# Kernel tuning notes

Measured on AMD Instinct MI355X. Metric: run time of the kernel, lower is better.

## Reference

```python
import jax, jax.numpy as jnp
import numpy as np

B, H, W, C = 2, 128, 128, 256
D = 64          # attention_dim
NH = 1          # num_heads
P = 18          # num_random_points
N = H * W
EPS = 1e-5


def _layernorm(x, gamma, beta):
    mu = jnp.mean(x, axis=-1, keepdims=True)
    var = jnp.var(x, axis=-1, keepdims=True)
    return (x - mu) * jax.lax.rsqrt(var + EPS) * gamma + beta


def setup_inputs() -> dict:
    key = jax.random.key(0)
    ks = jax.random.split(key, 12)
    s = 0.02
    inp = {
        "X": jax.random.normal(ks[0], (B, H, W, C), dtype=jnp.float32),
        "selected_indices": jax.random.randint(ks[1], (B, N, P), 0, N),
        "topk": 1,
        "pos_enc": jax.random.normal(ks[2], (1, H, W, C), dtype=jnp.float32),
        "Wq": jax.random.normal(ks[3], (C, NH * D), dtype=jnp.float32) * s,
        "bq": jnp.zeros((NH * D,), dtype=jnp.float32),
        "Wk": jax.random.normal(ks[4], (C, NH * D), dtype=jnp.float32) * s,
        "bk": jnp.zeros((NH * D,), dtype=jnp.float32),
        "Wv": jax.random.normal(ks[5], (C, NH * D), dtype=jnp.float32) * s,
        "bv": jnp.zeros((NH * D,), dtype=jnp.float32),
        "Wo": jax.random.normal(ks[6], (NH * D, C), dtype=jnp.float32) * s,
        "bo": jnp.zeros((C,), dtype=jnp.float32),
        "W1": jax.random.normal(ks[7], (C, 4 * C), dtype=jnp.float32) * s,
        "b1": jnp.zeros((4 * C,), dtype=jnp.float32),
        "W2": jax.random.normal(ks[8], (4 * C, C), dtype=jnp.float32) * s,
        "b2": jnp.zeros((C,), dtype=jnp.float32),
        "g1": jnp.ones((C,), dtype=jnp.float32),
        "be1": jnp.zeros((C,), dtype=jnp.float32),
        "g2": jnp.ones((C,), dtype=jnp.float32),
        "be2": jnp.zeros((C,), dtype=jnp.float32),
    }
    return inp


def reference(X, selected_indices, topk, pos_enc, Wq, bq, Wk, bk, Wv, bv,
              Wo, bo, W1, b1, W2, b2, g1, be1, g2, be2):
    # forward_wotopk path (topk == 1)
    Xp = X + pos_enc                                  # [B,H,W,C]
    Q = (Xp @ Wq + bq).reshape(B, N, NH, D)
    K = (Xp @ Wk + bk).reshape(B, N, NH, D)
    V = (Xp @ Wv + bv).reshape(B, N, NH, D)

    # gather 18 random K/V rows per query pixel: [B,N,P,NH,D]
    gather = jax.vmap(lambda kv, idx: kv[idx])        # per-batch fancy index
    Ksel = gather(K, selected_indices)
    Vsel = gather(V, selected_indices)

    scores = jnp.einsum('bihd,bijhd->bijh', Q, Ksel) / jnp.sqrt(
        jnp.asarray(D, dtype=jnp.float32))
    attn = jax.nn.softmax(scores, axis=2)             # softmax over the P points
    ctx = jnp.einsum('bijh,bijhd->bihd', attn, Vsel).reshape(B, N, NH * D)

    out = (ctx @ Wo + bo).reshape(B, H, W, C)
    Xn = _layernorm(Xp + out, g1, be1)
    ffn = jax.nn.relu(Xn @ W1 + b1) @ W2 + b2
    out2 = _layernorm(Xn + ffn, g2, be2)
    return out2, attn
```

## Files before the change

kernel.cpp:

```cpp
#include <hip/hip_runtime.h>
#include <hip/hip_bf16.h>

#define CC 256
#define DD 64
#define PP 18
#define ROWS 32768
#define EPSF 1e-5f

typedef __attribute__((ext_vector_type(8))) short bf16x8;
typedef __attribute__((ext_vector_type(4))) short s16x4;
typedef __attribute__((ext_vector_type(4))) float f32x4;

#define BAR_LDS() do {                                        \
    asm volatile("s_waitcnt lgkmcnt(0)" ::: "memory");        \
    __builtin_amdgcn_s_barrier();                             \
    __builtin_amdgcn_sched_barrier(0);                        \
} while (0)

__global__ __launch_bounds__(256) void k_prep(
    const float* __restrict__ Wq, const float* __restrict__ Wk,
    const float* __restrict__ Wv, const float* __restrict__ Wo,
    const float* __restrict__ W1, const float* __restrict__ W2,
    __hip_bfloat16* __restrict__ WqP, __hip_bfloat16* __restrict__ WkP,
    __hip_bfloat16* __restrict__ WvP, __hip_bfloat16* __restrict__ WoP,
    __hip_bfloat16* __restrict__ W1T, __hip_bfloat16* __restrict__ W2T) {
    __shared__ float tile[32][33];
    const int b = blockIdx.x, t = threadIdx.x;
    if (b < 256) {
        int i = b * 256 + t;
        const float* src; __hip_bfloat16* dst; int K, N, j;
        if (i < 16384)      { src = Wq; dst = WqP; K = 256; N = 64;  j = i; }
        else if (i < 32768) { src = Wk; dst = WkP; K = 256; N = 64;  j = i - 16384; }
        else if (i < 49152) { src = Wv; dst = WvP; K = 256; N = 64;  j = i - 32768; }
        else                { src = Wo; dst = WoP; K = 64;  N = 256; j = i - 49152; }
        int e = j & 7, l = (j >> 3) & 63, rest = j >> 9;
        int KS = K >> 5;
        int ks = rest % KS, nt = rest / KS;
        int row = ks * 32 + (l >> 4) * 8 + e;
        int col = nt * 16 + (l & 15);
        dst[j] = __float2bfloat16(src[(long)row * N + col]);
        return;
    }
    const float* src; __hip_bfloat16* dst; int Nsrc, r0, c0, mode;
    if (b < 512) {
        int bb = b - 256;
        r0 = (bb >> 5) * 32; c0 = (bb & 31) * 32;
        src = W1; dst = W1T; Nsrc = 1024; mode = 0;
    } else {
        int bb = b - 512;
        r0 = (bb >> 3) * 32; c0 = (bb & 7) * 32;
        src = W2; dst = W2T; Nsrc = 256; mode = 1;
    }
#pragma unroll
    for (int i = 0; i < 4; ++i) {
        int idx = t + i * 256;
        int r = idx >> 5, c = idx & 31;
        tile[r][c] = src[(long)(r0 + r) * Nsrc + c0 + c];
    }
    __syncthreads();
#pragma unroll
    for (int i = 0; i < 4; ++i) {
        int idx = t + i * 256;
        int c2 = idx >> 5, r2 = idx & 31;
        long doff = (mode == 0) ? ((long)(c0 + c2) * 256 + r0 + r2)
                                : ((long)(c0 + c2) * 1024 + r0 + r2);
        dst[doff] = __float2bfloat16(tile[r2][c2]);
    }
}

__global__ __launch_bounds__(256) void k_qkv(
    const float4* __restrict__ X4, const float4* __restrict__ pe4,
    const __hip_bfloat16* __restrict__ WqP, const __hip_bfloat16* __restrict__ WkP,
    const __hip_bfloat16* __restrict__ WvP,
    const float* __restrict__ bq, const float* __restrict__ bk,
    const float* __restrict__ bv,
    __hip_bfloat16* __restrict__ Xpb,
    __hip_bfloat16* __restrict__ Qb, __hip_bfloat16* __restrict__ Kb,
    __hip_bfloat16* __restrict__ Vb) {
    __shared__ short Xs[32 * 256];
    const int t = threadIdx.x, w = t >> 6, l = t & 63;
    const int l15 = l & 15, lh = l >> 4;
    const int row0 = blockIdx.x * 32;

    for (int j = t; j < 2048; j += 256) {
        int r = j >> 6, c4 = j & 63;
        long g = row0 + r;
        float4 a = X4[(g << 6) + c4];
        float4 p = pe4[(long)((g & 16383) << 6) + c4];
        union { s16x4 v; __hip_bfloat16 h[4]; } u;
        u.h[0] = __float2bfloat16(a.x + p.x);
        u.h[1] = __float2bfloat16(a.y + p.y);
        u.h[2] = __float2bfloat16(a.z + p.z);
        u.h[3] = __float2bfloat16(a.w + p.w);
        int db = (r << 9) + (c4 << 3);
        db ^= (r & 7) << 4;
        *(s16x4*)((char*)Xs + db) = u.v;
        *(s16x4*)((char*)Xpb + (g << 9) + (c4 << 3)) = u.v;
    }
    __syncthreads();

    bf16x8 af[2][8];
#pragma unroll
    for (int ri = 0; ri < 2; ++ri)
#pragma unroll
        for (int ks = 0; ks < 8; ++ks) {
            int r = ri * 16 + l15;
            int db = (r << 9) + ks * 64 + lh * 16;
            db ^= (r & 7) << 4;
            af[ri][ks] = *(const bf16x8*)((const char*)Xs + db);
        }

    f32x4 acc[3][2];
#pragma unroll
    for (int j = 0; j < 3; ++j)
#pragma unroll
        for (int ri = 0; ri < 2; ++ri) acc[j][ri] = (f32x4)(0.f);

#pragma unroll
    for (int ks = 0; ks < 8; ++ks)
#pragma unroll
        for (int j = 0; j < 3; ++j) {
            int nt = w * 3 + j;
            const __hip_bfloat16* WP = (nt < 4) ? WqP : ((nt < 8) ? WkP : WvP);
            int ntl = nt & 3;
            bf16x8 b = *(const bf16x8*)(WP + (long)(((ntl * 8 + ks) << 6) + l) * 8);
#pragma unroll
            for (int ri = 0; ri < 2; ++ri)
                acc[j][ri] = __builtin_amdgcn_mfma_f32_16x16x32_bf16(
                    af[ri][ks], b, acc[j][ri], 0, 0, 0);
        }

#pragma unroll
    for (int j = 0; j < 3; ++j) {
        int nt = w * 3 + j;
        __hip_bfloat16* OP = (nt < 4) ? Qb : ((nt < 8) ? Kb : Vb);
        const float* BP = (nt < 4) ? bq : ((nt < 8) ? bk : bv);
        int col = (nt & 3) * 16 + l15;
        float bias = BP[col];
#pragma unroll
        for (int ri = 0; ri < 2; ++ri)
#pragma unroll
            for (int rg = 0; rg < 4; ++rg) {
                long row = row0 + ri * 16 + lh * 4 + rg;
                OP[row * DD + col] = __float2bfloat16(acc[j][ri][rg] + bias);
            }
    }
}

__global__ __launch_bounds__(256) void k_attn(const __hip_bfloat16* __restrict__ Q,
                                              const __hip_bfloat16* __restrict__ K,
                                              const __hip_bfloat16* __restrict__ V,
                                              const int* __restrict__ sel,
                                              __hip_bfloat16* __restrict__ ctx,
                                              float* __restrict__ attn_out) {
    const int wave  = threadIdx.x >> 6;
    const int lane  = threadIdx.x & 63;
    const int token = blockIdx.x * 4 + wave;
    const int b     = token >> 14;
    const int g = lane >> 3, s = lane & 7;

    const int* selp = sel + (long)token * PP;
    int sel_l = (lane < PP) ? selp[lane] : 0;

    float qf[8];
    {
        uint4 qv = *(const uint4*)(Q + (long)token * DD + s * 8);
        qf[0] = __uint_as_float(qv.x << 16);
        qf[1] = __uint_as_float(qv.x & 0xffff0000u);
        qf[2] = __uint_as_float(qv.y << 16);
        qf[3] = __uint_as_float(qv.y & 0xffff0000u);
        qf[4] = __uint_as_float(qv.z << 16);
        qf[5] = __uint_as_float(qv.z & 0xffff0000u);
        qf[6] = __uint_as_float(qv.w << 16);
        qf[7] = __uint_as_float(qv.w & 0xffff0000u);
    }

    const __hip_bfloat16* Kbase = K + (((long)b << 14) * DD);
    float sc[3];
    int idxs[3];
#pragma unroll
    for (int i = 0; i < 3; ++i) {
        int r = i * 8 + g;
        idxs[i] = __shfl(sel_l, r);
        uint4 kv = *(const uint4*)(Kbase + (long)idxs[i] * DD + s * 8);
        float part;
        part = qf[0] * __uint_as_float(kv.x << 16);
        part = fmaf(qf[1], __uint_as_float(kv.x & 0xffff0000u), part);
        part = fmaf(qf[2], __uint_as_float(kv.y << 16), part);
        part = fmaf(qf[3], __uint_as_float(kv.y & 0xffff0000u), part);
        part = fmaf(qf[4], __uint_as_float(kv.z << 16), part);
        part = fmaf(qf[5], __uint_as_float(kv.z & 0xffff0000u), part);
        part = fmaf(qf[6], __uint_as_float(kv.w << 16), part);
        part = fmaf(qf[7], __uint_as_float(kv.w & 0xffff0000u), part);
        part += __shfl_xor(part, 1);
        part += __shfl_xor(part, 2);
        part += __shfl_xor(part, 4);
        sc[i] = (r < PP) ? part * 0.125f : -1e30f;
    }

    float m = fmaxf(fmaxf(sc[0], sc[1]), sc[2]);
    m = fmaxf(m, __shfl_xor(m, 8));
    m = fmaxf(m, __shfl_xor(m, 16));
    m = fmaxf(m, __shfl_xor(m, 32));
    const float L2E = 1.4426950408889634f;
    float e0 = exp2f((sc[0] - m) * L2E);
    float e1 = exp2f((sc[1] - m) * L2E);
    float e2 = exp2f((sc[2] - m) * L2E);
    float dsum = e0 + e1 + e2;
    dsum += __shfl_xor(dsum, 8);
    dsum += __shfl_xor(dsum, 16);
    dsum += __shfl_xor(dsum, 32);
    float inv = 1.f / dsum;

    {
        int srcl = (lane & 7) << 3;
        float b0 = __shfl(e0, srcl);
        float b1 = __shfl(e1, srcl);
        float b2 = __shfl(e2, srcl);
        if (lane < PP) {
            float ev = (lane < 8) ? b0 : ((lane < 16) ? b1 : b2);
            attn_out[(long)token * PP + lane] = ev * inv;
        }
    }

    const __hip_bfloat16* Vbase = V + (((long)b << 14) * DD);
    float ca[8];
#pragma unroll
    for (int j = 0; j < 8; ++j) ca[j] = 0.f;
    float ev3[3] = {e0, e1, e2};
#pragma unroll
    for (int i = 0; i < 3; ++i) {
        uint4 vv = *(const uint4*)(Vbase + (long)idxs[i] * DD + s * 8);
        float e = ev3[i];
        ca[0] = fmaf(e, __uint_as_float(vv.x << 16), ca[0]);
        ca[1] = fmaf(e, __uint_as_float(vv.x & 0xffff0000u), ca[1]);
        ca[2] = fmaf(e, __uint_as_float(vv.y << 16), ca[2]);
        ca[3] = fmaf(e, __uint_as_float(vv.y & 0xffff0000u), ca[3]);
        ca[4] = fmaf(e, __uint_as_float(vv.z << 16), ca[4]);
        ca[5] = fmaf(e, __uint_as_float(vv.z & 0xffff0000u), ca[5]);
        ca[6] = fmaf(e, __uint_as_float(vv.w << 16), ca[6]);
        ca[7] = fmaf(e, __uint_as_float(vv.w & 0xffff0000u), ca[7]);
    }
#pragma unroll
    for (int o = 8; o <= 32; o <<= 1)
#pragma unroll
        for (int j = 0; j < 8; ++j) ca[j] += __shfl_xor(ca[j], o);
    if (g == 0) {
        union { bf16x8 v; __hip_bfloat16 h[8]; } u;
#pragma unroll
        for (int j = 0; j < 8; ++j) u.h[j] = __float2bfloat16(ca[j] * inv);
        *(bf16x8*)(ctx + (long)token * DD + s * 8) = u.v;
    }
}

__global__ __launch_bounds__(256) void k_projln(
    const __hip_bfloat16* __restrict__ ctx, const __hip_bfloat16* __restrict__ WoP,
    const float* __restrict__ bo, const float* __restrict__ g1,
    const float* __restrict__ be1,
    const __hip_bfloat16* __restrict__ Xpb, __hip_bfloat16* __restrict__ Xnb) {
    __shared__ short Cs[32 * 64];
    __shared__ float red[2][32][2];
    __shared__ float mrs[32][2];
    const int t = threadIdx.x, w = t >> 6, l = t & 63;
    const int l15 = l & 15, lh = l >> 4;
    const int row0 = blockIdx.x * 32;

    {
        int r = t >> 3, ch = t & 7;
        int db = (r << 7) + (ch << 4);
        db ^= (r & 7) << 4;
        *(bf16x8*)((char*)Cs + db) = *(const bf16x8*)(ctx + (long)(row0 + r) * DD + ch * 8);
    }
    __syncthreads();

    const int ri = w & 1, nh = w >> 1;

    bf16x8 af[2];
#pragma unroll
    for (int ks = 0; ks < 2; ++ks) {
        int r = ri * 16 + l15;
        int db = (r << 7) + ks * 64 + lh * 16;
        db ^= (r & 7) << 4;
        af[ks] = *(const bf16x8*)((const char*)Cs + db);
    }

    f32x4 acc[8];
#pragma unroll
    for (int j = 0; j < 8; ++j) acc[j] = (f32x4)(0.f);

#pragma unroll
    for (int ks = 0; ks < 2; ++ks)
#pragma unroll
        for (int j = 0; j < 8; ++j) {
            int nt = nh * 8 + j;
            bf16x8 b = *(const bf16x8*)(WoP + (long)(((nt * 2 + ks) << 6) + l) * 8);
            acc[j] = __builtin_amdgcn_mfma_f32_16x16x32_bf16(af[ks], b, acc[j], 0, 0, 0);
        }

    float bov[8], g1v[8], be1v[8];
#pragma unroll
    for (int j = 0; j < 8; ++j) {
        int col = (nh * 8 + j) * 16 + l15;
        bov[j] = bo[col]; g1v[j] = g1[col]; be1v[j] = be1[col];
    }

    float xv[4][8];
#pragma unroll
    for (int rg = 0; rg < 4; ++rg) {
        long grow = row0 + ri * 16 + lh * 4 + rg;
        float s = 0.f, q = 0.f;
#pragma unroll
        for (int j = 0; j < 8; ++j) {
            float v = acc[j][rg] + bov[j] +
                      __bfloat162float(Xpb[grow * CC + (nh * 8 + j) * 16 + l15]);
            xv[rg][j] = v; s += v; q += v * v;
        }
#pragma unroll
        for (int o = 8; o > 0; o >>= 1) { s += __shfl_xor(s, o); q += __shfl_xor(q, o); }
        if (l15 == 0) {
            int rl = ri * 16 + lh * 4 + rg;
            red[nh][rl][0] = s; red[nh][rl][1] = q;
        }
    }
    __syncthreads();
    if (t < 32) {
        float S = red[0][t][0] + red[1][t][0];
        float Q = red[0][t][1] + red[1][t][1];
        float mu = S * (1.f / CC);
        float var = Q * (1.f / CC) - mu * mu;
        mrs[t][0] = mu; mrs[t][1] = rsqrtf(var + EPSF);
    }
    __syncthreads();
#pragma unroll
    for (int rg = 0; rg < 4; ++rg) {
        int rl = ri * 16 + lh * 4 + rg;
        long grow = row0 + rl;
        float mu = mrs[rl][0], rs = mrs[rl][1];
#pragma unroll
        for (int j = 0; j < 8; ++j)
            Xnb[grow * CC + (nh * 8 + j) * 16 + l15] =
                __float2bfloat16((xv[rg][j] - mu) * rs * g1v[j] + be1v[j]);
    }
}

template<int KD, int NDIM, int GRL2, int CTL2>
__global__ __launch_bounds__(256) void k_gemm(
    const __hip_bfloat16* __restrict__ A,
    const __hip_bfloat16* __restrict__ BT,
    const float* __restrict__ bias,
    __hip_bfloat16* __restrict__ Cout) {
    __shared__ short As[4096];
    __shared__ short Bs[4096];

    const int t = threadIdx.x, w = t >> 6, l = t & 63;
    const int l15 = l & 15, lh = l >> 4;
    const int bid = blockIdx.x;
    const int wi = bid & ((1 << (GRL2 + CTL2)) - 1);
    const int rt = ((bid >> (GRL2 + CTL2)) << GRL2) | (wi & ((1 << GRL2) - 1));
    const int ct = wi >> GRL2;
    const int row0 = rt * 128, n0 = ct * 128;
    const int wr = w & 1, wc = w >> 1;

    const int ar = t >> 2;
    const int ak = (t & 3) << 3;
    const int dbase = (ar * 64 + ((t & 3) << 4)) ^ ((ar & 7) << 4);
    const __hip_bfloat16* Ap = A + (long)(row0 + ar) * KD + ak;
    const __hip_bfloat16* Bp = BT + (long)(n0 + ar) * KD + ak;

    bf16x8 ra0 = *(const bf16x8*)(Ap);
    bf16x8 ra1 = *(const bf16x8*)(Ap + (long)64 * KD);
    bf16x8 rb0 = *(const bf16x8*)(Bp);
    bf16x8 rb1 = *(const bf16x8*)(Bp + (long)64 * KD);

    int offA[4], offB[4];
#pragma unroll
    for (int f = 0; f < 4; ++f) {
        int rowA = wr * 64 + f * 16 + l15;
        offA[f] = (rowA * 64 + lh * 16) ^ ((rowA & 7) << 4);
        int rowB = wc * 64 + f * 16 + l15;
        offB[f] = (rowB * 64 + lh * 16) ^ ((rowB & 7) << 4);
    }

    f32x4 acc[4][4];
#pragma unroll
    for (int i = 0; i < 4; ++i)
#pragma unroll
        for (int j = 0; j < 4; ++j) acc[i][j] = (f32x4)(0.f);

    constexpr int KS = KD / 32;
#pragma unroll 1
    for (int ks = 0; ks < KS; ++ks) {
        BAR_LDS();
        *(bf16x8*)((char*)As + dbase)        = ra0;
        *(bf16x8*)((char*)As + 4096 + dbase) = ra1;
        *(bf16x8*)((char*)Bs + dbase)        = rb0;
        *(bf16x8*)((char*)Bs + 4096 + dbase) = rb1;
        if (ks + 1 < KS) {
            const __hip_bfloat16* Ap2 = Ap + (ks + 1) * 32;
            const __hip_bfloat16* Bp2 = Bp + (ks + 1) * 32;
            ra0 = *(const bf16x8*)(Ap2);
            ra1 = *(const bf16x8*)(Ap2 + (long)64 * KD);
            rb0 = *(const bf16x8*)(Bp2);
            rb1 = *(const bf16x8*)(Bp2 + (long)64 * KD);
        }
        BAR_LDS();
        bf16x8 af[4], bfr[4];
#pragma unroll
        for (int f = 0; f < 4; ++f)
            af[f] = *(const bf16x8*)((const char*)As + offA[f]);
#pragma unroll
        for (int f = 0; f < 4; ++f)
            bfr[f] = *(const bf16x8*)((const char*)Bs + offB[f]);
#pragma unroll
        for (int fr = 0; fr < 4; ++fr)
#pragma unroll
            for (int fc = 0; fc < 4; ++fc)
                acc[fr][fc] = __builtin_amdgcn_mfma_f32_16x16x32_bf16(
                    af[fr], bfr[fc], acc[fr][fc], 0, 0, 0);
    }

#pragma unroll
    for (int fc = 0; fc < 4; ++fc) {
        int col = n0 + wc * 64 + fc * 16 + l15;
        float bv = bias[col];
#pragma unroll
        for (int fr = 0; fr < 4; ++fr)
#pragma unroll
            for (int rg = 0; rg < 4; ++rg) {
                int row = wr * 64 + fr * 16 + lh * 4 + rg;
                long gi = (long)(row0 + row) * NDIM + col;
                Cout[gi] = __float2bfloat16(fmaxf(acc[fr][fc][rg] + bv, 0.f));
            }
    }
}

__global__ __launch_bounds__(512) void k_gemm2ln(
    const __hip_bfloat16* __restrict__ A,
    const __hip_bfloat16* __restrict__ BT,
    const float* __restrict__ b2,
    const __hip_bfloat16* __restrict__ Res,
    const float* __restrict__ g2, const float* __restrict__ be2,
    float* __restrict__ out) {
    __shared__ short As[64 * 32];
    __shared__ short Bs[256 * 32];
    __shared__ float red[4][64][2];
    __shared__ float mrs[64][2];

    const int t = threadIdx.x, w = t >> 6, l = t & 63;
    const int l15 = l & 15, lh = l >> 4;
    const int wr = w >> 2, wc = w & 3;
    const int row0 = blockIdx.x * 64;
    const bool doA = (t < 256);

    const int ak = (t & 3) << 3;
    const int dbA  = ((t >> 2) * 64 + ((t & 3) << 4)) ^ (((t >> 2) & 7) << 4);
    const int brB0 = t >> 2;
    const int brB1 = brB0 + 128;
    const int dbB0 = (brB0 * 64 + ((t & 3) << 4)) ^ ((brB0 & 7) << 4);
    const int dbB1 = (brB1 * 64 + ((t & 3) << 4)) ^ ((brB1 & 7) << 4);
    const __hip_bfloat16* Ap  = A  + (long)(row0 + (t >> 2)) * 1024 + ak;
    const __hip_bfloat16* Bp0 = BT + (long)brB0 * 1024 + ak;
    const __hip_bfloat16* Bp1 = BT + (long)brB1 * 1024 + ak;

    bf16x8 ra;
    if (doA) ra = *(const bf16x8*)(Ap);
    bf16x8 rb0 = *(const bf16x8*)(Bp0);
    bf16x8 rb1 = *(const bf16x8*)(Bp1);

    int offA[2], offB[4];
#pragma unroll
    for (int f = 0; f < 2; ++f) {
        int rowA = wr * 32 + f * 16 + l15;
        offA[f] = (rowA * 64 + lh * 16) ^ ((rowA & 7) << 4);
    }
#pragma unroll
    for (int f = 0; f < 4; ++f) {
        int rowB = wc * 64 + f * 16 + l15;
        offB[f] = (rowB * 64 + lh * 16) ^ ((rowB & 7) << 4);
    }

    f32x4 acc[2][4];
#pragma unroll
    for (int i = 0; i < 2; ++i)
#pragma unroll
        for (int j = 0; j < 4; ++j) acc[i][j] = (f32x4)(0.f);

#pragma unroll 1
    for (int ks = 0; ks < 32; ++ks) {
        BAR_LDS();
        if (doA) *(bf16x8*)((char*)As + dbA) = ra;
        *(bf16x8*)((char*)Bs + dbB0) = rb0;
        *(bf16x8*)((char*)Bs + dbB1) = rb1;
        if (ks + 1 < 32) {
            if (doA) ra = *(const bf16x8*)(Ap + (ks + 1) * 32);
            rb0 = *(const bf16x8*)(Bp0 + (ks + 1) * 32);
            rb1 = *(const bf16x8*)(Bp1 + (ks + 1) * 32);
        }
        BAR_LDS();
        bf16x8 af[2], bfr[4];
#pragma unroll
        for (int f = 0; f < 2; ++f)
            af[f] = *(const bf16x8*)((const char*)As + offA[f]);
#pragma unroll
        for (int f = 0; f < 4; ++f)
            bfr[f] = *(const bf16x8*)((const char*)Bs + offB[f]);
#pragma unroll
        for (int fr = 0; fr < 2; ++fr)
#pragma unroll
            for (int fc = 0; fc < 4; ++fc)
                acc[fr][fc] = __builtin_amdgcn_mfma_f32_16x16x32_bf16(
                    af[fr], bfr[fc], acc[fr][fc], 0, 0, 0);
    }

    float b2v[4], g2v[4], be2v[4];
#pragma unroll
    for (int fc = 0; fc < 4; ++fc) {
        int col = wc * 64 + fc * 16 + l15;
        b2v[fc] = b2[col]; g2v[fc] = g2[col]; be2v[fc] = be2[col];
    }
#pragma unroll
    for (int fr = 0; fr < 2; ++fr)
#pragma unroll
        for (int rg = 0; rg < 4; ++rg) {
            int row = wr * 32 + fr * 16 + lh * 4 + rg;
            float s = 0.f, q = 0.f;
#pragma unroll
            for (int fc = 0; fc < 4; ++fc) {
                long gi = (long)(row0 + row) * CC + wc * 64 + fc * 16 + l15;
                float v = acc[fr][fc][rg] + b2v[fc] + __bfloat162float(Res[gi]);
                acc[fr][fc][rg] = v;
                s += v; q += v * v;
            }
#pragma unroll
            for (int o = 8; o > 0; o >>= 1) {
                s += __shfl_xor(s, o); q += __shfl_xor(q, o);
            }
            if (l15 == 0) { red[wc][row][0] = s; red[wc][row][1] = q; }
        }
    __syncthreads();
    if (t < 64) {
        float S = 0.f, Q = 0.f;
#pragma unroll
        for (int ww = 0; ww < 4; ++ww) { S += red[ww][t][0]; Q += red[ww][t][1]; }
        float mu = S * (1.f / CC);
        float var = Q * (1.f / CC) - mu * mu;
        mrs[t][0] = mu; mrs[t][1] = rsqrtf(var + EPSF);
    }
    __syncthreads();
#pragma unroll
    for (int fr = 0; fr < 2; ++fr)
#pragma unroll
        for (int rg = 0; rg < 4; ++rg) {
            int row = wr * 32 + fr * 16 + lh * 4 + rg;
            float mu = mrs[row][0], rs = mrs[row][1];
#pragma unroll
            for (int fc = 0; fc < 4; ++fc) {
                long gi = (long)(row0 + row) * CC + wc * 64 + fc * 16 + l15;
                out[gi] = (acc[fr][fc][rg] - mu) * rs * g2v[fc] + be2v[fc];
            }
        }
}

extern "C" void kernel_launch(void* const* d_in, const int* in_sizes, int n_in,
                              void* d_out, int out_size, void* d_ws, size_t ws_size,
                              hipStream_t stream) {
    const float* X   = (const float*)d_in[0];
    const int*   sel = (const int*)d_in[1];
    const float* pe  = (const float*)d_in[3];
    const float* Wq  = (const float*)d_in[4];
    const float* bq  = (const float*)d_in[5];
    const float* Wk  = (const float*)d_in[6];
    const float* bk  = (const float*)d_in[7];
    const float* Wv  = (const float*)d_in[8];
    const float* bv  = (const float*)d_in[9];
    const float* Wo  = (const float*)d_in[10];
    const float* bo  = (const float*)d_in[11];
    const float* W1  = (const float*)d_in[12];
    const float* b1  = (const float*)d_in[13];
    const float* W2  = (const float*)d_in[14];
    const float* b2  = (const float*)d_in[15];
    const float* g1  = (const float*)d_in[16];
    const float* be1 = (const float*)d_in[17];
    const float* g2  = (const float*)d_in[18];
    const float* be2 = (const float*)d_in[19];

    float* out = (float*)d_out;
    char*  ws  = (char*)d_ws;

    __hip_bfloat16* Xpb = (__hip_bfloat16*)(ws);
    __hip_bfloat16* Qb  = (__hip_bfloat16*)(ws + (16 << 20));
    __hip_bfloat16* Kb  = (__hip_bfloat16*)(ws + (20 << 20));
    __hip_bfloat16* Vb  = (__hip_bfloat16*)(ws + (24 << 20));
    __hip_bfloat16* ctxb= (__hip_bfloat16*)(ws + (28 << 20));
    __hip_bfloat16* H   = (__hip_bfloat16*)(ws + (16 << 20));
    __hip_bfloat16* WqP = (__hip_bfloat16*)(ws + (96 << 20));
    __hip_bfloat16* WkP = WqP + 16384;
    __hip_bfloat16* WvP = WkP + 16384;
    __hip_bfloat16* WoP = WvP + 16384;
    __hip_bfloat16* W1T = WoP + 16384;
    __hip_bfloat16* W2T = W1T + 262144;
    float* attn_out = out + (long)ROWS * CC;

    k_prep<<<768, 256, 0, stream>>>(Wq, Wk, Wv, Wo, W1, W2,
                                    WqP, WkP, WvP, WoP, W1T, W2T);

    k_qkv<<<ROWS / 32, 256, 0, stream>>>((const float4*)X, (const float4*)pe,
                                         WqP, WkP, WvP, bq, bk, bv,
                                         Xpb, Qb, Kb, Vb);

    k_attn<<<ROWS / 4, 256, 0, stream>>>(Qb, Kb, Vb, sel, ctxb, attn_out);

    k_projln<<<ROWS / 32, 256, 0, stream>>>(ctxb, WoP, bo, g1, be1, Xpb, Xpb);

    k_gemm<256, 1024, 3, 3><<<2048, 256, 0, stream>>>(Xpb, W1T, b1, H);
    k_gemm2ln<<<512, 512, 0, stream>>>(H, W2T, b2, Xpb, g2, be2, out);
}
```

Measured before the change: 119.5 us.

## Use direct global-to-LDS loads with double-buffered pipeline in FFN GEMMs

Replaces the register-staged global loads and LDS stores in the two FFN GEMM kernels with global_load_lds (direct-to-LDS DMA) into a two-stage LDS ring. Prefetch runs two K-steps ahead and is synchronised with vmcnt waits instead of two LDS barriers per step. An inverse swizzle maps each lane's LDS destination back to its global source so the existing XOR-swizzled fragment reads keep working. The aim is to drop the VGPR staging and LDS write instructions and to overlap memory with MFMA work. In exchange it doubles LDS use, which may lower occupancy, and it depends on correct vmcnt accounting.

```diff
diff --git a/kernel.cpp b/kernel.cpp
--- a/kernel.cpp
+++ b/kernel.cpp
@@ -16,6 +16,26 @@
     __builtin_amdgcn_s_barrier();                             \
     __builtin_amdgcn_sched_barrier(0);                        \
 } while (0)
+
+#define WAIT_VM(N) do {                                       \
+    asm volatile("s_waitcnt vmcnt(" #N ")" ::: "memory");     \
+    __builtin_amdgcn_s_barrier();                             \
+    __builtin_amdgcn_sched_barrier(0);                        \
+} while (0)
+
+__device__ __forceinline__ void gl_lds16(const void* g, void* l) {
+    __builtin_amdgcn_global_load_lds(
+        (const __attribute__((address_space(1))) unsigned int*)g,
+        (__attribute__((address_space(3))) unsigned int*)l, 16, 0, 0);
+}
+
+__device__ __forceinline__ void inv_swz(int p, int& r, int& c) {
+    int rhi = p >> 7;
+    int r2  = (rhi >> 1) & 1;
+    int r0  = ((p >> 6) & 1) ^ r2;
+    r = (rhi << 1) | r0;
+    c = ((p >> 4) & 3) ^ (r & 3);
+}
 
 __global__ __launch_bounds__(256) void k_prep(
     const float* __restrict__ Wq, const float* __restrict__ Wk,
@@ -349,8 +369,8 @@
     const __hip_bfloat16* __restrict__ BT,
     const float* __restrict__ bias,
     __hip_bfloat16* __restrict__ Cout) {
-    __shared__ short As[4096];
-    __shared__ short Bs[4096];
+    __shared__ short As[2][4096];
+    __shared__ short Bs[2][4096];
 
     const int t = threadIdx.x, w = t >> 6, l = t & 63;
     const int l15 = l & 15, lh = l >> 4;
@@ -361,16 +381,17 @@
     const int row0 = rt * 128, n0 = ct * 128;
     const int wr = w & 1, wc = w >> 1;
 
-    const int ar = t >> 2;
-    const int ak = (t & 3) << 3;
-    const int dbase = (ar * 64 + ((t & 3) << 4)) ^ ((ar & 7) << 4);
-    const __hip_bfloat16* Ap = A + (long)(row0 + ar) * KD + ak;
-    const __hip_bfloat16* Bp = BT + (long)(n0 + ar) * KD + ak;
-
-    bf16x8 ra0 = *(const bf16x8*)(Ap);
-    bf16x8 ra1 = *(const bf16x8*)(Ap + (long)64 * KD);
-    bf16x8 rb0 = *(const bf16x8*)(Bp);
-    bf16x8 rb1 = *(const bf16x8*)(Bp + (long)64 * KD);
+    const __hip_bfloat16* gA[2];
+    const __hip_bfloat16* gB[2];
+#pragma unroll
+    for (int j = 0; j < 2; ++j) {
+        int r, c;
+        inv_swz(j * 4096 + t * 16, r, c);
+        gA[j] = A  + (long)(row0 + r) * KD + c * 8;
+        gB[j] = BT + (long)(n0 + r) * KD + c * 8;
+    }
+    char* ldsA = (char*)As + w * 1024;
+    char* ldsB = (char*)Bs + w * 1024;
 
     int offA[4], offB[4];
 #pragma unroll
@@ -388,35 +409,41 @@
         for (int j = 0; j < 4; ++j) acc[i][j] = (f32x4)(0.f);
 
     constexpr int KS = KD / 32;
+#pragma unroll
+    for (int n = 0; n < 2; ++n)
+#pragma unroll
+        for (int j = 0; j < 2; ++j) {
+            gl_lds16(gA[j] + n * 32, ldsA + n * 8192 + j * 4096);
+            gl_lds16(gB[j] + n * 32, ldsB + n * 8192 + j * 4096);
+        }
+
 #pragma unroll 1
     for (int ks = 0; ks < KS; ++ks) {
-        BAR_LDS();
-        *(bf16x8*)((char*)As + dbase)        = ra0;
-        *(bf16x8*)((char*)As + 4096 + dbase) = ra1;
-        *(bf16x8*)((char*)Bs + dbase)        = rb0;
-        *(bf16x8*)((char*)Bs + 4096 + dbase) = rb1;
-        if (ks + 1 < KS) {
-            const __hip_bfloat16* Ap2 = Ap + (ks + 1) * 32;
-            const __hip_bfloat16* Bp2 = Bp + (ks + 1) * 32;
-            ra0 = *(const bf16x8*)(Ap2);
-            ra1 = *(const bf16x8*)(Ap2 + (long)64 * KD);
-            rb0 = *(const bf16x8*)(Bp2);
-            rb1 = *(const bf16x8*)(Bp2 + (long)64 * KD);
-        }
-        BAR_LDS();
+        if (ks + 1 < KS) { WAIT_VM(4); } else { WAIT_VM(0); }
+        const char* as = (const char*)As + (ks & 1) * 8192;
+        const char* bs = (const char*)Bs + (ks & 1) * 8192;
         bf16x8 af[4], bfr[4];
 #pragma unroll
         for (int f = 0; f < 4; ++f)
-            af[f] = *(const bf16x8*)((const char*)As + offA[f]);
+            af[f] = *(const bf16x8*)(as + offA[f]);
 #pragma unroll
         for (int f = 0; f < 4; ++f)
-            bfr[f] = *(const bf16x8*)((const char*)Bs + offB[f]);
+            bfr[f] = *(const bf16x8*)(bs + offB[f]);
 #pragma unroll
         for (int fr = 0; fr < 4; ++fr)
 #pragma unroll
             for (int fc = 0; fc < 4; ++fc)
                 acc[fr][fc] = __builtin_amdgcn_mfma_f32_16x16x32_bf16(
                     af[fr], bfr[fc], acc[fr][fc], 0, 0, 0);
+        BAR_LDS();
+        if (ks + 2 < KS) {
+            int n = ks + 2;
+#pragma unroll
+            for (int j = 0; j < 2; ++j) {
+                gl_lds16(gA[j] + n * 32, ldsA + (ks & 1) * 8192 + j * 4096);
+                gl_lds16(gB[j] + n * 32, ldsB + (ks & 1) * 8192 + j * 4096);
+            }
+        }
     }
 
 #pragma unroll
@@ -441,8 +468,8 @@
     const __hip_bfloat16* __restrict__ Res,
     const float* __restrict__ g2, const float* __restrict__ be2,
     float* __restrict__ out) {
-    __shared__ short As[64 * 32];
-    __shared__ short Bs[256 * 32];
+    __shared__ short As[2][2048];
+    __shared__ short Bs[2][8192];
     __shared__ float red[4][64][2];
     __shared__ float mrs[64][2];
 
@@ -452,20 +479,21 @@
     const int row0 = blockIdx.x * 64;
     const bool doA = (t < 256);
 
-    const int ak = (t & 3) << 3;
-    const int dbA  = ((t >> 2) * 64 + ((t & 3) << 4)) ^ (((t >> 2) & 7) << 4);
-    const int brB0 = t >> 2;
-    const int brB1 = brB0 + 128;
-    const int dbB0 = (brB0 * 64 + ((t & 3) << 4)) ^ ((brB0 & 7) << 4);
-    const int dbB1 = (brB1 * 64 + ((t & 3) << 4)) ^ ((brB1 & 7) << 4);
-    const __hip_bfloat16* Ap  = A  + (long)(row0 + (t >> 2)) * 1024 + ak;
-    const __hip_bfloat16* Bp0 = BT + (long)brB0 * 1024 + ak;
-    const __hip_bfloat16* Bp1 = BT + (long)brB1 * 1024 + ak;
-
-    bf16x8 ra;
-    if (doA) ra = *(const bf16x8*)(Ap);
-    bf16x8 rb0 = *(const bf16x8*)(Bp0);
-    bf16x8 rb1 = *(const bf16x8*)(Bp1);
+    const __hip_bfloat16* gA = A;
+    {
+        int r, c;
+        inv_swz((t & 255) * 16, r, c);
+        gA = A + (long)(row0 + r) * 1024 + c * 8;
+    }
+    const __hip_bfloat16* gB[2];
+#pragma unroll
+    for (int j = 0; j < 2; ++j) {
+        int r, c;
+        inv_swz(j * 8192 + t * 16, r, c);
+        gB[j] = BT + (long)r * 1024 + c * 8;
+    }
+    char* ldsA = (char*)As + (w & 3) * 1024;
+    char* ldsB = (char*)Bs + w * 1024;
 
     int offA[2], offB[4];
 #pragma unroll
@@ -485,31 +513,44 @@
 #pragma unroll
         for (int j = 0; j < 4; ++j) acc[i][j] = (f32x4)(0.f);
 
+#pragma unroll
+    for (int n = 0; n < 2; ++n) {
+        if (doA) gl_lds16(gA + n * 32, ldsA + n * 4096);
+#pragma unroll
+        for (int j = 0; j < 2; ++j)
+            gl_lds16(gB[j] + n * 32, ldsB + n * 16384 + j * 8192);
+    }
+
 #pragma unroll 1
     for (int ks = 0; ks < 32; ++ks) {
-        BAR_LDS();
-        if (doA) *(bf16x8*)((char*)As + dbA) = ra;
-        *(bf16x8*)((char*)Bs + dbB0) = rb0;
-        *(bf16x8*)((char*)Bs + dbB1) = rb1;
         if (ks + 1 < 32) {
-            if (doA) ra = *(const bf16x8*)(Ap + (ks + 1) * 32);
-            rb0 = *(const bf16x8*)(Bp0 + (ks + 1) * 32);
-            rb1 = *(const bf16x8*)(Bp1 + (ks + 1) * 32);
-        }
-        BAR_LDS();
+            if (doA) { WAIT_VM(3); } else { WAIT_VM(2); }
+        } else {
+            WAIT_VM(0);
+        }
+        const char* as = (const char*)As + (ks & 1) * 4096;
+        const char* bs = (const char*)Bs + (ks & 1) * 16384;
         bf16x8 af[2], bfr[4];
 #pragma unroll
         for (int f = 0; f < 2; ++f)
-            af[f] = *(const bf16x8*)((const char*)As + offA[f]);
+            af[f] = *(const bf16x8*)(as + offA[f]);
 #pragma unroll
         for (int f = 0; f < 4; ++f)
-            bfr[f] = *(const bf16x8*)((const char*)Bs + offB[f]);
+            bfr[f] = *(const bf16x8*)(bs + offB[f]);
 #pragma unroll
         for (int fr = 0; fr < 2; ++fr)
 #pragma unroll
             for (int fc = 0; fc < 4; ++fc)
                 acc[fr][fc] = __builtin_amdgcn_mfma_f32_16x16x32_bf16(
                     af[fr], bfr[fc], acc[fr][fc], 0, 0, 0);
+        BAR_LDS();
+        if (ks + 2 < 32) {
+            int n = ks + 2;
+            if (doA) gl_lds16(gA + n * 32, ldsA + (ks & 1) * 4096);
+#pragma unroll
+            for (int j = 0; j < 2; ++j)
+                gl_lds16(gB[j] + n * 32, ldsB + (ks & 1) * 16384 + j * 8192);
+        }
     }
 
     float b2v[4], g2v[4], be2v[4];
```

Result: no change. 120.3 us (+0.6%).
